# Kernel tuning notes

Measured on AMD Instinct MI355X. Metric: run time of the kernel, lower is better.

## Reference

```python
import jax, jax.numpy as jnp
import numpy as np

D_GNN, D_MODEL = 512, 2048
B, T = 4, 4096
EPS = 1e-5


def layer_norm(x, gamma, beta):
    mu = jnp.mean(x, axis=-1, keepdims=True)
    var = jnp.mean(jnp.square(x - mu), axis=-1, keepdims=True)
    return (x - mu) * jax.lax.rsqrt(var + EPS) * gamma + beta


def setup_inputs() -> dict:
    key = jax.random.key(0)
    ks = jax.random.split(key, 10)
    s_proj = 1.0 / np.sqrt(D_GNN)
    s_mod = 1.0 / np.sqrt(D_MODEL)
    s_gate = 1.0 / np.sqrt(2 * D_MODEL)
    return {
        "h_llm": jax.random.normal(ks[0], (B, T, D_MODEL), jnp.float32),
        "h_change": jax.random.normal(ks[1], (B, D_GNN), jnp.float32),
        # h_change_proj: Linear(d_gnn -> d_model)
        "w_proj": jax.random.uniform(ks[2], (D_MODEL, D_GNN), jnp.float32, -s_proj, s_proj),
        "b_proj": jnp.zeros((D_MODEL,), jnp.float32),
        "g1": jnp.ones((D_MODEL,), jnp.float32),
        "b1": jnp.zeros((D_MODEL,), jnp.float32),
        # MHA value / output projections (q,k are mathematically irrelevant: kv_len==1 -> softmax==1)
        "w_v": jax.random.uniform(ks[3], (D_MODEL, D_MODEL), jnp.float32, -s_mod, s_mod),
        "b_v": jnp.zeros((D_MODEL,), jnp.float32),
        "w_o": jax.random.uniform(ks[4], (D_MODEL, D_MODEL), jnp.float32, -s_mod, s_mod),
        "b_o": jnp.zeros((D_MODEL,), jnp.float32),
        "g2": jnp.ones((D_MODEL,), jnp.float32),
        "b2": jnp.zeros((D_MODEL,), jnp.float32),
        # fusion gate: Linear(2*d_model -> d_model) + sigmoid
        "w_gate": jax.random.uniform(ks[5], (D_MODEL, 2 * D_MODEL), jnp.float32, -s_gate, s_gate),
        "b_gate": jnp.zeros((D_MODEL,), jnp.float32),
        "g3": jnp.ones((D_MODEL,), jnp.float32),
        "b3": jnp.zeros((D_MODEL,), jnp.float32),
    }


def reference(h_llm, h_change, w_proj, b_proj, g1, b1, w_v, b_v, w_o, b_o,
              g2, b2, w_gate, b_gate, g3, b3):
    # project GNN feature to d_model, then LayerNorm  -> (B, D)
    hc = layer_norm(h_change @ w_proj.T + b_proj, g1, b1)
    # cross-attention with kv_len == 1: softmax over a single key is identically 1,
    # so attn_output == out_proj(value_proj(hc)), broadcast over T. Dropout is eval (identity).
    attn = (hc @ w_v.T + b_v) @ w_o.T + b_o                 # (B, D)
    attn_out = layer_norm(h_llm + attn[:, None, :], g2, b2)  # (B, T, D)
    # gated residual fusion: gate = sigmoid(W [h_llm ; attn_out] + b)
    wg_l, wg_a = w_gate[:, :D_MODEL], w_gate[:, D_MODEL:]
    gate = jax.nn.sigmoid(h_llm @ wg_l.T + attn_out @ wg_a.T + b_gate)
    fused = gate * attn_out + (1.0 - gate) * h_llm
    return layer_norm(fused, g3, b3)
```

## Files before the change

kernel.cpp:

```cpp
#include <hip/hip_runtime.h>
#include <hip/hip_bf16.h>
#include <cstdint>
#include <cstddef>

#define DM 2048
#define DG 512
#define NBATCH 4
#define NT 4096
#define NM (NBATCH*NT)
#define KC (2*DM)
#define LN_EPS 1e-5f
#define NTILES (KC/128)
#define SCL_A 16.0f
#define SCL_B 8192.0f
#define DESCALE (1.0f/131072.0f)

typedef __bf16 bf16;
typedef bf16 bf16x8 __attribute__((ext_vector_type(8)));
typedef float f32x4 __attribute__((ext_vector_type(4)));
typedef int   i32x4 __attribute__((ext_vector_type(4)));
typedef char  i8x8  __attribute__((ext_vector_type(8)));
typedef unsigned char u8x8 __attribute__((ext_vector_type(8)));

#define AS1 __attribute__((address_space(1)))
#define AS3 __attribute__((address_space(3)))

__device__ __forceinline__ char q8(float x, float s) {
    int v = (int)rintf(x * s);
    v = v > 127 ? 127 : (v < -127 ? -127 : v);
    return (char)v;
}

__device__ __forceinline__ void block_reduce_2(float& s, float& s2) {
#pragma unroll
    for (int off = 32; off; off >>= 1) {
        s  += __shfl_down(s, off);
        s2 += __shfl_down(s2, off);
    }
    __shared__ float sm[8];
    const int wid = threadIdx.x >> 6, lane = threadIdx.x & 63;
    if (lane == 0) { sm[wid] = s; sm[4 + wid] = s2; }
    __syncthreads();
    s  = sm[0] + sm[1] + sm[2] + sm[3];
    s2 = sm[4] + sm[5] + sm[6] + sm[7];
}

__global__ void k_cvt_i8(const float* __restrict__ src, int8_t* __restrict__ dst, int n8) {
    int i = blockIdx.x * blockDim.x + threadIdx.x;
    if (i >= n8) return;
    const f32x4* s = (const f32x4*)src + (size_t)i * 2;
    f32x4 a = s[0], b = s[1];
    i8x8 o;
#pragma unroll
    for (int q = 0; q < 4; q++) { o[q] = q8(a[q], SCL_B); o[4+q] = q8(b[q], SCL_B); }
    *((i8x8*)dst + i) = o;
}

template<int K>
__global__ void k_dot(const float* __restrict__ X, const float* __restrict__ W,
                      const float* __restrict__ bias, float* __restrict__ out) {
    const int lane = threadIdx.x & 63;
    const int wid  = threadIdx.x >> 6;
    const int j = blockIdx.x * 4 + wid;
    const f32x4* Wr = (const f32x4*)(W + (size_t)j * K);
    float acc[NBATCH] = {0.f, 0.f, 0.f, 0.f};
    constexpr int C = K / 4 / 64;
#pragma unroll
    for (int i = 0; i < C; i++) {
        f32x4 wv = Wr[lane + 64 * i];
#pragma unroll
        for (int b = 0; b < NBATCH; b++) {
            f32x4 xv = ((const f32x4*)(X + (size_t)b * K))[lane + 64 * i];
            acc[b] += wv[0]*xv[0] + wv[1]*xv[1] + wv[2]*xv[2] + wv[3]*xv[3];
        }
    }
#pragma unroll
    for (int off = 32; off; off >>= 1)
#pragma unroll
        for (int b = 0; b < NBATCH; b++) acc[b] += __shfl_down(acc[b], off);
    if (lane == 0) {
        const float bb = bias[j];
#pragma unroll
        for (int b = 0; b < NBATCH; b++) out[(size_t)b * DM + j] = acc[b] + bb;
    }
}

__global__ void k_ln_small(const float* __restrict__ in, const float* __restrict__ g,
                           const float* __restrict__ bt, float* __restrict__ out) {
    const int row = blockIdx.x;
    const int tid = threadIdx.x;
    const f32x4* ir = (const f32x4*)(in + (size_t)row * DM);
    f32x4 v0 = ir[tid], v1 = ir[tid + 256];
    float s  = v0[0]+v0[1]+v0[2]+v0[3] + v1[0]+v1[1]+v1[2]+v1[3];
    float s2 = v0[0]*v0[0]+v0[1]*v0[1]+v0[2]*v0[2]+v0[3]*v0[3]
             + v1[0]*v1[0]+v1[1]*v1[1]+v1[2]*v1[2]+v1[3]*v1[3];
    block_reduce_2(s, s2);
    const float mu = s * (1.0f / DM);
    const float r  = rsqrtf(s2 * (1.0f / DM) - mu * mu + LN_EPS);
    f32x4 g0 = ((const f32x4*)g)[tid],  g1v = ((const f32x4*)g)[tid + 256];
    f32x4 b0 = ((const f32x4*)bt)[tid], b1v = ((const f32x4*)bt)[tid + 256];
    f32x4 o0 = (v0 - mu) * r * g0 + b0;
    f32x4 o1 = (v1 - mu) * r * g1v + b1v;
    f32x4* orow = (f32x4*)(out + (size_t)row * DM);
    orow[tid] = o0; orow[tid + 256] = o1;
}

__global__ void k_stats_pack(const float* __restrict__ h, const float* __restrict__ attnv,
                             const float* __restrict__ g2, const float* __restrict__ b2,
                             int8_t* __restrict__ Aq, bf16* __restrict__ hbf,
                             float* __restrict__ muA, float* __restrict__ rA) {
    const int m = blockIdx.x;
    const int b = m >> 12;
    const int tid = threadIdx.x;
    const f32x4* hr = (const f32x4*)(h + (size_t)m * DM);
    const f32x4* ar = (const f32x4*)(attnv + (size_t)b * DM);
    f32x4 h0 = hr[2*tid], h1 = hr[2*tid + 1];
    f32x4 a0 = ar[2*tid], a1 = ar[2*tid + 1];
    f32x4 x0 = h0 + a0, x1 = h1 + a1;
    float s  = x0[0]+x0[1]+x0[2]+x0[3] + x1[0]+x1[1]+x1[2]+x1[3];
    float s2 = x0[0]*x0[0]+x0[1]*x0[1]+x0[2]*x0[2]+x0[3]*x0[3]
             + x1[0]*x1[0]+x1[1]*x1[1]+x1[2]*x1[2]+x1[3]*x1[3];
    block_reduce_2(s, s2);
    const float mu = s * (1.0f / DM);
    const float r  = rsqrtf(s2 * (1.0f / DM) - mu * mu + LN_EPS);
    if (tid == 0) { muA[m] = mu; rA[m] = r; }
    f32x4 gg0 = ((const f32x4*)g2)[2*tid], gg1 = ((const f32x4*)g2)[2*tid + 1];
    f32x4 bb0 = ((const f32x4*)b2)[2*tid], bb1 = ((const f32x4*)b2)[2*tid + 1];
    f32x4 ao0 = (x0 - mu) * r * gg0 + bb0;
    f32x4 ao1 = (x1 - mu) * r * gg1 + bb1;
    bf16x8 hv;
#pragma unroll
    for (int q = 0; q < 4; q++) { hv[q] = (bf16)h0[q]; hv[4+q] = (bf16)h1[q]; }
    *(bf16x8*)(hbf + (size_t)m * DM + 8*tid) = hv;
    i8x8 qh, qa;
#pragma unroll
    for (int q = 0; q < 4; q++) {
        qh[q] = q8(h0[q], SCL_A);  qh[4+q] = q8(h1[q], SCL_A);
        qa[q] = q8(ao0[q], SCL_A); qa[4+q] = q8(ao1[q], SCL_A);
    }
    *(i8x8*)(Aq + (size_t)m * KC + 8*tid) = qh;
    *(i8x8*)(Aq + (size_t)m * KC + DM + 8*tid) = qa;
}

#define MF(a,b,c) __builtin_amdgcn_mfma_i32_16x16x64_i8(a,b,c,0,0,0)
#define SCHED0() __builtin_amdgcn_sched_barrier(0)
#define BAR()  { SCHED0(); asm volatile("s_barrier" ::: "memory"); SCHED0(); }
#define VM(n)  { asm volatile("s_waitcnt vmcnt(" #n ")" ::: "memory"); SCHED0(); }
#define LGKM(n) { asm volatile("s_waitcnt lgkmcnt(" #n ")" ::: "memory"); SCHED0(); }

__global__ __launch_bounds__(512, 2) void k_gemm256(const int8_t* __restrict__ A, const int8_t* __restrict__ Bw,
                                                    const float* __restrict__ bgate, uint8_t* __restrict__ gq) {
    __shared__ __align__(128) char smem[131072];
    const int tid  = threadIdx.x;
    const int lane = tid & 63;
    const int wid  = tid >> 6;
    const int wm   = wid >> 2, wn = wid & 3;

    const int swz = (blockIdx.x & 7) * 64 + (blockIdx.x >> 3);
    const int bm = (swz >> 3) << 8;
    const int bn = (swz & 7) << 8;

    const int r_local = tid >> 3;
    const int sc = (tid & 7) ^ (r_local & 7);
    const int8_t* Abase = A  + (size_t)(bm + r_local) * KC + sc*16;
    const int8_t* Bbase = Bw + (size_t)(bn + r_local) * KC + sc*16;
    const int ldsW = wid << 10;

#define STAGEA(buf, rnd, kt) __builtin_amdgcn_global_load_lds( \
        (const AS1 void*)(Abase + (size_t)(rnd)*64*KC + (kt)*128), \
        (AS3 void*)(smem + (buf)*65536 + (rnd)*8192 + ldsW), 16, 0, 0)
#define STAGEB(buf, rnd, kt) __builtin_amdgcn_global_load_lds( \
        (const AS1 void*)(Bbase + (size_t)(rnd)*64*KC + (kt)*128), \
        (AS3 void*)(smem + (buf)*65536 + 32768 + (rnd)*8192 + ldsW), 16, 0, 0)

    const int co0 = ((lane >> 4) ^ (lane & 7)) << 4;
    const int co1 = ((4 + (lane >> 4)) ^ (lane & 7)) << 4;
    const int arowb = (wm*128 + (lane & 15)) * 128;
    const int browb = (wn*64  + (lane & 15)) * 128;

#define AFRG(buf, m, ks) (*(const i32x4*)(smem + (buf)*65536 + arowb + (m)*2048 + ((ks) ? co1 : co0)))
#define BFRG(buf, n, ks) (*(const i32x4*)(smem + (buf)*65536 + 32768 + browb + (n)*2048 + ((ks) ? co1 : co0)))

    i32x4 acc[8][4] = {};
    i32x4 aLo[4][2], aHi[4][2], b01[2][2], b23[2][2];

#define LOAD_ALO(buf) { _Pragma("unroll") for (int i = 0; i < 4; i++) { aLo[i][0] = AFRG(buf,i,0);   aLo[i][1] = AFRG(buf,i,1);   } }
#define LOAD_AHI(buf) { _Pragma("unroll") for (int i = 0; i < 4; i++) { aHi[i][0] = AFRG(buf,4+i,0); aHi[i][1] = AFRG(buf,4+i,1); } }
#define LOAD_B01(buf) { _Pragma("unroll") for (int j = 0; j < 2; j++) { b01[j][0] = BFRG(buf,j,0);   b01[j][1] = BFRG(buf,j,1);   } }
#define LOAD_B23(buf) { _Pragma("unroll") for (int j = 0; j < 2; j++) { b23[j][0] = BFRG(buf,2+j,0); b23[j][1] = BFRG(buf,2+j,1); } }

#define MMQ(MOFF, AF, BF, NOFF) { _Pragma("unroll") for (int i = 0; i < 4; i++) \
        _Pragma("unroll") for (int j = 0; j < 2; j++) { \
            acc[(MOFF)+i][(NOFF)+j] = MF(AF[i][0], BF[j][0], acc[(MOFF)+i][(NOFF)+j]); \
            acc[(MOFF)+i][(NOFF)+j] = MF(AF[i][1], BF[j][1], acc[(MOFF)+i][(NOFF)+j]); } }

    STAGEB(0,0,0); STAGEB(0,1,0); STAGEB(0,2,0); STAGEB(0,3,0);
    STAGEA(0,0,0); STAGEA(0,2,0); STAGEA(0,1,0); STAGEA(0,3,0);
    VM(0);
    BAR();

#define TILE_BODY(TT, BUF, NBUF) { \
    const bool g = (TT) < NTILES - 1; \
     \
    if (g) { STAGEB(NBUF,0,(TT)+1); STAGEB(NBUF,1,(TT)+1); STAGEB(NBUF,2,(TT)+1); STAGEB(NBUF,3,(TT)+1); } \
    LOAD_ALO(BUF); LOAD_B01(BUF); LOAD_B23(BUF); SCHED0(); \
    LGKM(4); \
    __builtin_amdgcn_s_setprio(1); \
    MMQ(0, aLo, b01, 0); \
    __builtin_amdgcn_s_setprio(0); SCHED0(); \
     \
    if (g) { STAGEA(NBUF,0,(TT)+1); STAGEA(NBUF,1,(TT)+1); STAGEA(NBUF,2,(TT)+1); STAGEA(NBUF,3,(TT)+1); } \
    LOAD_AHI(BUF); SCHED0(); \
    LGKM(8); \
    __builtin_amdgcn_s_setprio(1); \
    MMQ(0, aLo, b23, 2); \
    __builtin_amdgcn_s_setprio(0); SCHED0(); \
     \
    LGKM(0); \
    __builtin_amdgcn_s_setprio(1); \
    MMQ(4, aHi, b23, 2); \
    __builtin_amdgcn_s_setprio(0); SCHED0(); \
     \
    __builtin_amdgcn_s_setprio(1); \
    MMQ(4, aHi, b01, 0); \
    __builtin_amdgcn_s_setprio(0); SCHED0(); \
    VM(0); \
    BAR(); \
}

    for (int T = 0; T < NTILES; T += 2) {
        TILE_BODY(T,   0, 1);
        TILE_BODY(T+1, 1, 0);
    }

#pragma unroll
    for (int n = 0; n < 4; n++) {
        const int col = bn + wn*64 + n*16 + (lane & 15);
        const float bg = bgate[col];
#pragma unroll
        for (int m = 0; m < 8; m++) {
            const int row = bm + wm*128 + m*16 + ((lane >> 4) << 2);
#pragma unroll
            for (int r = 0; r < 4; r++) {
                const float z = (float)acc[m][n][r] * DESCALE + bg;
                const float gate = 1.0f / (1.0f + __expf(-z));
                gq[(size_t)(row + r) * DM + col] = (uint8_t)(int)rintf(gate * 255.0f);
            }
        }
    }
}

__global__ void k_epilogue(const bf16* __restrict__ hbf, const uint8_t* __restrict__ gq,
                           const float* __restrict__ attnv, const float* __restrict__ muA,
                           const float* __restrict__ rA,
                           const float* __restrict__ g2, const float* __restrict__ b2,
                           const float* __restrict__ g3, const float* __restrict__ b3,
                           float* __restrict__ out) {
    const int m = blockIdx.x;
    const int b = m >> 12;
    const int tid = threadIdx.x;
    bf16x8 hb = *(const bf16x8*)(hbf + (size_t)m * DM + 8*tid);
    f32x4 h0, h1;
#pragma unroll
    for (int q = 0; q < 4; q++) { h0[q] = (float)hb[q]; h1[q] = (float)hb[4+q]; }
    const f32x4* ar = (const f32x4*)(attnv + (size_t)b * DM);
    f32x4 a0 = ar[2*tid], a1 = ar[2*tid + 1];
    const float mu = muA[m];
    const float r  = rA[m];
    f32x4 gg0 = ((const f32x4*)g2)[2*tid], gg1 = ((const f32x4*)g2)[2*tid + 1];
    f32x4 bb0 = ((const f32x4*)b2)[2*tid], bb1 = ((const f32x4*)b2)[2*tid + 1];
    f32x4 ao0 = (h0 + a0 - mu) * r * gg0 + bb0;
    f32x4 ao1 = (h1 + a1 - mu) * r * gg1 + bb1;
    u8x8 qv = *(const u8x8*)(gq + (size_t)m * DM + 8*tid);
    f32x4 gt0, gt1;
#pragma unroll
    for (int q = 0; q < 4; q++) {
        gt0[q] = (float)qv[q]   * (1.0f / 255.0f);
        gt1[q] = (float)qv[4+q] * (1.0f / 255.0f);
    }
    f32x4 f0 = h0 + gt0 * (ao0 - h0);
    f32x4 f1 = h1 + gt1 * (ao1 - h1);
    float s  = f0[0]+f0[1]+f0[2]+f0[3] + f1[0]+f1[1]+f1[2]+f1[3];
    float s2 = f0[0]*f0[0]+f0[1]*f0[1]+f0[2]*f0[2]+f0[3]*f0[3]
             + f1[0]*f1[0]+f1[1]*f1[1]+f1[2]*f1[2]+f1[3]*f1[3];
    block_reduce_2(s, s2);
    const float mu3 = s * (1.0f / DM);
    const float r3  = rsqrtf(s2 * (1.0f / DM) - mu3 * mu3 + LN_EPS);
    f32x4 g30 = ((const f32x4*)g3)[2*tid], g31 = ((const f32x4*)g3)[2*tid + 1];
    f32x4 b30 = ((const f32x4*)b3)[2*tid], b31 = ((const f32x4*)b3)[2*tid + 1];
    f32x4 o0 = (f0 - mu3) * r3 * g30 + b30;
    f32x4 o1 = (f1 - mu3) * r3 * g31 + b31;
    f32x4* orow = (f32x4*)(out + (size_t)m * DM);
    orow[2*tid] = o0; orow[2*tid + 1] = o1;
}

extern "C" void kernel_launch(void* const* d_in, const int* in_sizes, int n_in,
                              void* d_out, int out_size, void* d_ws, size_t ws_size,
                              hipStream_t stream) {
    const float* h_llm    = (const float*)d_in[0];
    const float* h_change = (const float*)d_in[1];
    const float* w_proj   = (const float*)d_in[2];
    const float* b_proj   = (const float*)d_in[3];
    const float* g1       = (const float*)d_in[4];
    const float* b1       = (const float*)d_in[5];
    const float* w_v      = (const float*)d_in[6];
    const float* b_v      = (const float*)d_in[7];
    const float* w_o      = (const float*)d_in[8];
    const float* b_o      = (const float*)d_in[9];
    const float* g2       = (const float*)d_in[10];
    const float* b2       = (const float*)d_in[11];
    const float* w_gate   = (const float*)d_in[12];
    const float* b_gate   = (const float*)d_in[13];
    const float* g3       = (const float*)d_in[14];
    const float* b3       = (const float*)d_in[15];
    float* out = (float*)d_out;

    char* ws = (char*)d_ws;
    int8_t* Aq  = (int8_t*)ws; ws += (size_t)NM * KC;
    int8_t* wqb = (int8_t*)ws; ws += (size_t)DM * KC;
    bf16* hbf = (bf16*)ws;    ws += (size_t)NM * DM * 2;
    uint8_t* gq = (uint8_t*)ws; ws += (size_t)NM * DM;
    float* muA = (float*)ws;  ws += (size_t)NM * 4;
    float* rA  = (float*)ws;  ws += (size_t)NM * 4;
    float* raw1 = (float*)ws; ws += (size_t)NBATCH * DM * 4;
    float* hc   = (float*)ws; ws += (size_t)NBATCH * DM * 4;
    float* raw2 = (float*)ws; ws += (size_t)NBATCH * DM * 4;
    float* attnv= (float*)ws; ws += (size_t)NBATCH * DM * 4;

    k_cvt_i8<<<(DM * KC / 8 + 255) / 256, 256, 0, stream>>>(w_gate, wqb, DM * KC / 8);
    k_dot<DG><<<DM / 4, 256, 0, stream>>>(h_change, w_proj, b_proj, raw1);
    k_ln_small<<<NBATCH, 256, 0, stream>>>(raw1, g1, b1, hc);
    k_dot<DM><<<DM / 4, 256, 0, stream>>>(hc, w_v, b_v, raw2);
    k_dot<DM><<<DM / 4, 256, 0, stream>>>(raw2, w_o, b_o, attnv);
    k_stats_pack<<<NM, 256, 0, stream>>>(h_llm, attnv, g2, b2, Aq, hbf, muA, rA);
    k_gemm256<<<512, 512, 0, stream>>>(Aq, wqb, b_gate, gq);
    k_epilogue<<<NM, 256, 0, stream>>>(hbf, gq, attnv, muA, rA, g2, b2, g3, b3, out);
}
```

Measured before the change: 279.6 us.

## Prepack int8 gate weights in MFMA fragment order and load B directly to registers

The weight quantization kernel now writes w_gate in a layout matching the MFMA B-fragment order, so each lane reads its fragment with one contiguous 16-byte global load. The GEMM drops the LDS staging for B, halving shared memory to 64KB, and prefetches next-tile B fragments into registers between MFMA groups with reworked vmcnt waits. This removes LDS traffic and bank pressure for B, but each wave re-reads B from global/L2 with no sharing across the waves that use the same columns, and the waitcnt accounting is delicate.

```diff
diff --git a/kernel.cpp b/kernel.cpp
--- a/kernel.cpp
+++ b/kernel.cpp
@@ -20,6 +20,7 @@
 typedef float f32x4 __attribute__((ext_vector_type(4)));
 typedef int   i32x4 __attribute__((ext_vector_type(4)));
 typedef char  i8x8  __attribute__((ext_vector_type(8)));
+typedef char  i8x16 __attribute__((ext_vector_type(16)));
 typedef unsigned char u8x8 __attribute__((ext_vector_type(8)));
 
 #define AS1 __attribute__((address_space(1)))
@@ -45,15 +46,20 @@
     s2 = sm[4] + sm[5] + sm[6] + sm[7];
 }
 
-__global__ void k_cvt_i8(const float* __restrict__ src, int8_t* __restrict__ dst, int n8) {
-    int i = blockIdx.x * blockDim.x + threadIdx.x;
-    if (i >= n8) return;
-    const f32x4* s = (const f32x4*)src + (size_t)i * 2;
-    f32x4 a = s[0], b = s[1];
-    i8x8 o;
-#pragma unroll
-    for (int q = 0; q < 4; q++) { o[q] = q8(a[q], SCL_B); o[4+q] = q8(b[q], SCL_B); }
-    *((i8x8*)dst + i) = o;
+__global__ void k_pack_i8(const float* __restrict__ src, int8_t* __restrict__ dst) {
+    int t = blockIdx.x * blockDim.x + threadIdx.x;
+    const int lane = t & 63, ks = (t >> 6) & 1, kt = (t >> 7) & 31, col16 = t >> 12;
+    const int row = col16 * 16 + (lane & 15);
+    const int k0  = kt * 128 + ks * 64 + (lane >> 4) * 16;
+    const f32x4* s = (const f32x4*)(src + (size_t)row * KC + k0);
+    f32x4 a = s[0], b = s[1], c = s[2], d = s[3];
+    i8x16 o;
+#pragma unroll
+    for (int q = 0; q < 4; q++) {
+        o[q] = q8(a[q], SCL_B); o[4+q] = q8(b[q], SCL_B);
+        o[8+q] = q8(c[q], SCL_B); o[12+q] = q8(d[q], SCL_B);
+    }
+    *((i8x16*)dst + t) = o;
 }
 
 template<int K>
@@ -148,9 +154,9 @@
 #define VM(n)  { asm volatile("s_waitcnt vmcnt(" #n ")" ::: "memory"); SCHED0(); }
 #define LGKM(n) { asm volatile("s_waitcnt lgkmcnt(" #n ")" ::: "memory"); SCHED0(); }
 
-__global__ __launch_bounds__(512, 2) void k_gemm256(const int8_t* __restrict__ A, const int8_t* __restrict__ Bw,
+__global__ __launch_bounds__(512, 2) void k_gemm256(const int8_t* __restrict__ A, const int8_t* __restrict__ PB,
                                                     const float* __restrict__ bgate, uint8_t* __restrict__ gq) {
-    __shared__ __align__(128) char smem[131072];
+    __shared__ __align__(128) char smem[65536];
     const int tid  = threadIdx.x;
     const int lane = tid & 63;
     const int wid  = tid >> 6;
@@ -162,69 +168,77 @@
 
     const int r_local = tid >> 3;
     const int sc = (tid & 7) ^ (r_local & 7);
-    const int8_t* Abase = A  + (size_t)(bm + r_local) * KC + sc*16;
-    const int8_t* Bbase = Bw + (size_t)(bn + r_local) * KC + sc*16;
+    const int8_t* Abase = A + (size_t)(bm + r_local) * KC + sc*16;
     const int ldsW = wid << 10;
 
 #define STAGEA(buf, rnd, kt) __builtin_amdgcn_global_load_lds( \
         (const AS1 void*)(Abase + (size_t)(rnd)*64*KC + (kt)*128), \
-        (AS3 void*)(smem + (buf)*65536 + (rnd)*8192 + ldsW), 16, 0, 0)
-#define STAGEB(buf, rnd, kt) __builtin_amdgcn_global_load_lds( \
-        (const AS1 void*)(Bbase + (size_t)(rnd)*64*KC + (kt)*128), \
-        (AS3 void*)(smem + (buf)*65536 + 32768 + (rnd)*8192 + ldsW), 16, 0, 0)
+        (AS3 void*)(smem + (buf)*32768 + (rnd)*8192 + ldsW), 16, 0, 0)
 
     const int co0 = ((lane >> 4) ^ (lane & 7)) << 4;
     const int co1 = ((4 + (lane >> 4)) ^ (lane & 7)) << 4;
     const int arowb = (wm*128 + (lane & 15)) * 128;
-    const int browb = (wn*64  + (lane & 15)) * 128;
-
-#define AFRG(buf, m, ks) (*(const i32x4*)(smem + (buf)*65536 + arowb + (m)*2048 + ((ks) ? co1 : co0)))
-#define BFRG(buf, n, ks) (*(const i32x4*)(smem + (buf)*65536 + 32768 + browb + (n)*2048 + ((ks) ? co1 : co0)))
+
+#define AFRG(buf, m, ks) (*(const i32x4*)(smem + (buf)*32768 + arowb + (m)*2048 + ((ks) ? co1 : co0)))
+
+    const int8_t* PBp[4];
+#pragma unroll
+    for (int n = 0; n < 4; n++)
+        PBp[n] = PB + (size_t)((bn >> 4) + wn * 4 + n) * 65536 + lane * 16;
 
     i32x4 acc[8][4] = {};
     i32x4 aLo[4][2], aHi[4][2], b01[2][2], b23[2][2];
 
 #define LOAD_ALO(buf) { _Pragma("unroll") for (int i = 0; i < 4; i++) { aLo[i][0] = AFRG(buf,i,0);   aLo[i][1] = AFRG(buf,i,1);   } }
 #define LOAD_AHI(buf) { _Pragma("unroll") for (int i = 0; i < 4; i++) { aHi[i][0] = AFRG(buf,4+i,0); aHi[i][1] = AFRG(buf,4+i,1); } }
-#define LOAD_B01(buf) { _Pragma("unroll") for (int j = 0; j < 2; j++) { b01[j][0] = BFRG(buf,j,0);   b01[j][1] = BFRG(buf,j,1);   } }
-#define LOAD_B23(buf) { _Pragma("unroll") for (int j = 0; j < 2; j++) { b23[j][0] = BFRG(buf,2+j,0); b23[j][1] = BFRG(buf,2+j,1); } }
+#define LOADB01(kt) { _Pragma("unroll") for (int j = 0; j < 2; j++) { \
+        b01[j][0] = *(const i32x4*)(PBp[j]   + (kt)*2048);        \
+        b01[j][1] = *(const i32x4*)(PBp[j]   + (kt)*2048 + 1024); } }
+#define LOADB23(kt) { _Pragma("unroll") for (int j = 0; j < 2; j++) { \
+        b23[j][0] = *(const i32x4*)(PBp[2+j] + (kt)*2048);        \
+        b23[j][1] = *(const i32x4*)(PBp[2+j] + (kt)*2048 + 1024); } }
 
 #define MMQ(MOFF, AF, BF, NOFF) { _Pragma("unroll") for (int i = 0; i < 4; i++) \
         _Pragma("unroll") for (int j = 0; j < 2; j++) { \
             acc[(MOFF)+i][(NOFF)+j] = MF(AF[i][0], BF[j][0], acc[(MOFF)+i][(NOFF)+j]); \
             acc[(MOFF)+i][(NOFF)+j] = MF(AF[i][1], BF[j][1], acc[(MOFF)+i][(NOFF)+j]); } }
 
-    STAGEB(0,0,0); STAGEB(0,1,0); STAGEB(0,2,0); STAGEB(0,3,0);
-    STAGEA(0,0,0); STAGEA(0,2,0); STAGEA(0,1,0); STAGEA(0,3,0);
-    VM(0);
+    STAGEA(0,0,0); STAGEA(0,1,0); STAGEA(0,2,0); STAGEA(0,3,0);
+    LOADB01(0);
+    LOADB23(0);
+    VM(8);
     BAR();
 
 #define TILE_BODY(TT, BUF, NBUF) { \
     const bool g = (TT) < NTILES - 1; \
      \
-    if (g) { STAGEB(NBUF,0,(TT)+1); STAGEB(NBUF,1,(TT)+1); STAGEB(NBUF,2,(TT)+1); STAGEB(NBUF,3,(TT)+1); } \
-    LOAD_ALO(BUF); LOAD_B01(BUF); LOAD_B23(BUF); SCHED0(); \
-    LGKM(4); \
+    if (g) { STAGEA(NBUF,0,(TT)+1); STAGEA(NBUF,2,(TT)+1); } \
+    LOAD_ALO(BUF); SCHED0(); \
+    if (g) { VM(6); } else { VM(4); } \
+    LGKM(0); \
     __builtin_amdgcn_s_setprio(1); \
     MMQ(0, aLo, b01, 0); \
     __builtin_amdgcn_s_setprio(0); SCHED0(); \
      \
-    if (g) { STAGEA(NBUF,0,(TT)+1); STAGEA(NBUF,1,(TT)+1); STAGEA(NBUF,2,(TT)+1); STAGEA(NBUF,3,(TT)+1); } \
+    if (g) { STAGEA(NBUF,1,(TT)+1); STAGEA(NBUF,3,(TT)+1); } \
     LOAD_AHI(BUF); SCHED0(); \
-    LGKM(8); \
+    if (g) { VM(4); } else { VM(0); } \
     __builtin_amdgcn_s_setprio(1); \
     MMQ(0, aLo, b23, 2); \
     __builtin_amdgcn_s_setprio(0); SCHED0(); \
      \
     LGKM(0); \
     __builtin_amdgcn_s_setprio(1); \
+    MMQ(4, aHi, b01, 0); \
+    __builtin_amdgcn_s_setprio(0); \
+    if (g) { LOADB01((TT)+1); } SCHED0(); \
+     \
+    __builtin_amdgcn_s_setprio(1); \
     MMQ(4, aHi, b23, 2); \
-    __builtin_amdgcn_s_setprio(0); SCHED0(); \
-     \
-    __builtin_amdgcn_s_setprio(1); \
-    MMQ(4, aHi, b01, 0); \
-    __builtin_amdgcn_s_setprio(0); SCHED0(); \
-    VM(0); \
+    __builtin_amdgcn_s_setprio(0); \
+    if (g) { LOADB23((TT)+1); } SCHED0(); \
+     \
+    if (g) { VM(8); } \
     BAR(); \
 }
 
@@ -317,7 +331,7 @@
 
     char* ws = (char*)d_ws;
     int8_t* Aq  = (int8_t*)ws; ws += (size_t)NM * KC;
-    int8_t* wqb = (int8_t*)ws; ws += (size_t)DM * KC;
+    int8_t* PB  = (int8_t*)ws; ws += (size_t)DM * KC;
     bf16* hbf = (bf16*)ws;    ws += (size_t)NM * DM * 2;
     uint8_t* gq = (uint8_t*)ws; ws += (size_t)NM * DM;
     float* muA = (float*)ws;  ws += (size_t)NM * 4;
@@ -327,12 +341,12 @@
     float* raw2 = (float*)ws; ws += (size_t)NBATCH * DM * 4;
     float* attnv= (float*)ws; ws += (size_t)NBATCH * DM * 4;
 
-    k_cvt_i8<<<(DM * KC / 8 + 255) / 256, 256, 0, stream>>>(w_gate, wqb, DM * KC / 8);
+    k_pack_i8<<<2048, 256, 0, stream>>>(w_gate, PB);
     k_dot<DG><<<DM / 4, 256, 0, stream>>>(h_change, w_proj, b_proj, raw1);
     k_ln_small<<<NBATCH, 256, 0, stream>>>(raw1, g1, b1, hc);
     k_dot<DM><<<DM / 4, 256, 0, stream>>>(hc, w_v, b_v, raw2);
     k_dot<DM><<<DM / 4, 256, 0, stream>>>(raw2, w_o, b_o, attnv);
     k_stats_pack<<<NM, 256, 0, stream>>>(h_llm, attnv, g2, b2, Aq, hbf, muA, rA);
-    k_gemm256<<<512, 512, 0, stream>>>(Aq, wqb, b_gate, gq);
+    k_gemm256<<<512, 512, 0, stream>>>(Aq, PB, b_gate, gq);
     k_epilogue<<<NM, 256, 0, stream>>>(hbf, gq, attnv, muA, rA, g2, b2, g3, b3, out);
 }
```

Measured after the change: 286.6 us. 2.5% more time.
